# Performance work log

Measured on AMD Instinct MI355X. Metric: run time of the kernel, lower is better.

## Reference

```python
import jax, jax.numpy as jnp
import numpy as np

B, S, E, H = 2, 2048, 1024, 16
DH = E // H            # 64 head dim
ROT = DH // 2          # 32: RotaryEmbedding(head_dim//2) rotates first 32 dims only
CTX = 2048             # sliding KV window
THETA = 10000.0


def setup_inputs() -> dict:
    key = jax.random.key(0)
    ks = jax.random.split(key, 7)
    sc = 1.0 / np.sqrt(E)
    mk = lambda k, sh, s=1.0: (jax.random.normal(k, sh, jnp.float32) * s)
    return {
        "query": mk(ks[0], (B, S, E)),
        "key":   mk(ks[1], (B, S, E)),
        "value": mk(ks[2], (B, S, E)),
        "Wq": mk(ks[3], (E, E), sc), "bq": jnp.zeros((E,), jnp.float32),
        "Wk": mk(ks[4], (E, E), sc), "bk": jnp.zeros((E,), jnp.float32),
        "Wv": mk(ks[5], (E, E), sc), "bv": jnp.zeros((E,), jnp.float32),
        "Wo": mk(ks[6], (E, E), sc), "bo": jnp.zeros((E,), jnp.float32),
    }


def _rope(t):
    # t: [B, H, S, DH]; rotate first ROT dims, pass the rest through (offset=0).
    seq = t.shape[2]
    inv_freq = 1.0 / (THETA ** (jnp.arange(0, ROT, 2, dtype=jnp.float32) / ROT))  # [ROT//2]
    ang = jnp.arange(seq, dtype=jnp.float32)[:, None] * inv_freq[None, :]          # [S, ROT//2]
    cos = jnp.repeat(jnp.cos(ang), 2, axis=-1)  # [S, ROT] (pairwise-interleaved freqs)
    sin = jnp.repeat(jnp.sin(ang), 2, axis=-1)
    rot, rest = t[..., :ROT], t[..., ROT:]
    x1, x2 = rot[..., 0::2], rot[..., 1::2]
    rot_half = jnp.stack([-x2, x1], axis=-1).reshape(rot.shape)  # rotate_half on pairs
    return jnp.concatenate([rot * cos + rot_half * sin, rest], axis=-1)


def reference(query, key, value, Wq, bq, Wk, bk, Wv, bv, Wo, bo):
    def heads(x, W, b):
        return (x @ W.T + b).reshape(B, -1, H, DH).transpose(0, 2, 1, 3)  # [B,H,S,DH]

    q = _rope(heads(query, Wq, bq))
    k = _rope(heads(key, Wk, bk))
    v = heads(value, Wv, bv)
    k, v = k[:, :, -CTX:], v[:, :, -CTX:]  # sliding window (no-op when S == CTX)

    scale = jnp.float32(1.0 / np.sqrt(DH))
    scores = jnp.einsum('bhqd,bhkd->bhqk', q, k) * scale  # [B,H,Sq,Sk]
    sq, sk = q.shape[2], k.shape[2]
    causal = jnp.tril(jnp.ones((sk, sk), dtype=bool))[-sq:]  # [Sq,Sk]
    scores = jnp.where(causal[None, None], scores, jnp.float32(-jnp.inf))
    probs = jax.nn.softmax(scores, axis=-1)  # dropout=0 (eval)
    out = jnp.einsum('bhqk,bhkd->bhqd', probs, v)
    out = out.transpose(0, 2, 1, 3).reshape(B, -1, E)
    return out @ Wo.T + bo
```

## Files before the change

### kernel.cpp

```cpp
#include <hip/hip_runtime.h>
#include <stdint.h>
#include <math.h>

typedef __bf16 bf16x8 __attribute__((ext_vector_type(8)));
typedef float f32x4 __attribute__((ext_vector_type(4)));

__device__ __forceinline__ float bf2f(uint16_t x) {
  unsigned u = ((unsigned)x) << 16;
  float f;
  __builtin_memcpy(&f, &u, 4);
  return f;
}
__device__ __forceinline__ uint16_t f2bf(float f) {
  __bf16 h = (__bf16)f;
  uint16_t u;
  __builtin_memcpy(&u, &h, 2);
  return u;
}
__device__ __forceinline__ bf16x8 cvt8(const float* p) {
  const float4 lo = *(const float4*)p;
  const float4 hi = *(const float4*)(p + 4);
  bf16x8 v;
  v[0] = (__bf16)lo.x; v[1] = (__bf16)lo.y; v[2] = (__bf16)lo.z; v[3] = (__bf16)lo.w;
  v[4] = (__bf16)hi.x; v[5] = (__bf16)hi.y; v[6] = (__bf16)hi.z; v[7] = (__bf16)hi.w;
  return v;
}

typedef __attribute__((address_space(1))) const unsigned int gu32;
typedef __attribute__((address_space(3))) unsigned int lu32;
__device__ __forceinline__ void async_copy16(const void* gp, void* lp) {
  __builtin_amdgcn_global_load_lds((gu32*)gp, (lu32*)lp, 16, 0, 0);
}

__global__ __launch_bounds__(256) void cvt_kernel(
    const float* __restrict__ s0, uint16_t* __restrict__ d0,
    const float* __restrict__ s1, uint16_t* __restrict__ d1,
    const float* __restrict__ s2, uint16_t* __restrict__ d2) {
  const int z = blockIdx.z;
  const float* s = z == 0 ? s0 : z == 1 ? s1 : s2;
  uint16_t* d = z == 0 ? d0 : z == 1 ? d1 : d2;
  const size_t idx = ((size_t)blockIdx.x * 256 + threadIdx.x) * 8;
  *(bf16x8*)(d + idx) = cvt8(s + idx);
}

template <bool A_F32, bool W_F32, bool C_F32, bool VT>
__global__ __launch_bounds__(256) void gemm3_kernel(
    const void* __restrict__ A0, const void* __restrict__ W0,
    const float* __restrict__ b0, void* __restrict__ C0,
    const void* __restrict__ A1, const void* __restrict__ W1,
    const float* __restrict__ b1, void* __restrict__ C1,
    const void* __restrict__ A2, const void* __restrict__ W2,
    const float* __restrict__ b2, void* __restrict__ C2,
    int M, int N, int K) {
  const int z = blockIdx.z;
  const void* Av = z == 0 ? A0 : z == 1 ? A1 : A2;
  const void* Wp = z == 0 ? W0 : z == 1 ? W1 : W2;
  const float* bias = z == 0 ? b0 : z == 1 ? b1 : b2;
  void* Cv = z == 0 ? C0 : z == 1 ? C1 : C2;

  __shared__ __align__(16) uint16_t As[128 * 64];
  __shared__ __align__(16) uint16_t Bs[128 * 64];
  const int tid = threadIdx.x;
  const int wave = tid >> 6, lane = tid & 63;
  const int quad = lane >> 4, l16 = lane & 15;
  const int l = blockIdx.y * 8 + blockIdx.x;
  const int bn = (l >> 5) << 7;
  const int bm = (l & 31) << 7;
  const int wm = (wave >> 1) << 6, wn = (wave & 1) << 6;

  f32x4 acc[4][4] = {};

  for (int k0 = 0; k0 < K; k0 += 64) {
    bf16x8 ar[4], wr[4];
    if (A_F32) {
#pragma unroll
      for (int i = 0; i < 4; i++) {
        const int c = i * 256 + tid;
        const int r = c >> 3, pc = ((c & 7) ^ (r & 7)) << 3;
        ar[i] = cvt8((const float*)Av + (size_t)(bm + r) * K + k0 + pc);
      }
    }
    if (W_F32) {
#pragma unroll
      for (int i = 0; i < 4; i++) {
        const int c = i * 256 + tid;
        const int r = c >> 3, pc = ((c & 7) ^ (r & 7)) << 3;
        wr[i] = cvt8((const float*)Wp + (size_t)(bn + r) * K + k0 + pc);
      }
    }
    if (k0) __syncthreads();
#pragma unroll
    for (int i = 0; i < 4; i++) {
      const int c = i * 256 + tid;
      const int r = c >> 3, pc = ((c & 7) ^ (r & 7)) << 3;
      if (A_F32) *(bf16x8*)(As + c * 8) = ar[i];
      else async_copy16((const uint16_t*)Av + (size_t)(bm + r) * K + k0 + pc,
                        As + (i * 256 + (tid & 192)) * 8);
      if (W_F32) *(bf16x8*)(Bs + c * 8) = wr[i];
      else async_copy16((const uint16_t*)Wp + (size_t)(bn + r) * K + k0 + pc,
                        Bs + (i * 256 + (tid & 192)) * 8);
    }
    __syncthreads();
#pragma unroll
    for (int s = 0; s < 2; s++) {
      bf16x8 af[4], bfr[4];
#pragma unroll
      for (int i = 0; i < 4; i++) {
        const int Ra = wm + i * 16 + l16;
        af[i]  = *(const bf16x8*)(As + Ra * 64 + (((s * 4 + quad) ^ (Ra & 7)) << 3));
        const int Rb = wn + i * 16 + l16;
        bfr[i] = *(const bf16x8*)(Bs + Rb * 64 + (((s * 4 + quad) ^ (Rb & 7)) << 3));
      }
#pragma unroll
      for (int i = 0; i < 4; i++)
#pragma unroll
        for (int j = 0; j < 4; j++)
          acc[i][j] = __builtin_amdgcn_mfma_f32_16x16x32_bf16(af[i], bfr[j], acc[i][j], 0, 0, 0);
    }
  }
  if (VT && z == 2) {
#pragma unroll
    for (int j = 0; j < 4; j++) {
      const int n = bn + wn + j * 16 + l16;
      const float bj = bias[n];
      const int h = n >> 6, dh = n & 63;
#pragma unroll
      for (int i = 0; i < 4; i++) {
        const int m0 = bm + wm + i * 16 + quad * 4;
        const int b = m0 >> 11, s0 = m0 & 2047;
        uint2 pk;
        pk.x = (unsigned)f2bf(acc[i][j][0] + bj) |
               ((unsigned)f2bf(acc[i][j][1] + bj) << 16);
        pk.y = (unsigned)f2bf(acc[i][j][2] + bj) |
               ((unsigned)f2bf(acc[i][j][3] + bj) << 16);
        *(uint2*)((uint16_t*)Cv + ((size_t)((b * 16 + h) * 64 + dh)) * 2048 + s0) = pk;
      }
    }
  } else {
#pragma unroll
    for (int j = 0; j < 4; j++) {
      const int n = bn + wn + j * 16 + l16;
      const float bj = bias[n];
#pragma unroll
      for (int i = 0; i < 4; i++) {
        const int m0 = bm + wm + i * 16 + quad * 4;
#pragma unroll
        for (int r = 0; r < 4; r++) {
          const float v = acc[i][j][r] + bj;
          if (C_F32) ((float*)Cv)[(size_t)(m0 + r) * N + n] = v;
          else       ((uint16_t*)Cv)[(size_t)(m0 + r) * N + n] = f2bf(v);
        }
      }
    }
  }
}

__global__ __launch_bounds__(256) void rope_kernel(uint16_t* __restrict__ Q,
                                                   uint16_t* __restrict__ K) {
  const int tid = blockIdx.x * 256 + threadIdx.x;
  const int i = tid & 15;
  const int h = (tid >> 4) & 15;
  const int s = (tid >> 8) & 2047;
  const int b = tid >> 19;
  const size_t base = ((size_t)(b * 2048 + s) * 1024) + h * 64 + 2 * i;
  const float inv = __expf(-0.5756462732485115f * (float)i);
  float rev = ((float)s * inv) * 0.15915494309189535f;
  rev -= floorf(rev);
  const float sn = __builtin_amdgcn_sinf(rev);
  const float c  = __builtin_amdgcn_cosf(rev);
  {
    uint32_t p = *(const uint32_t*)(Q + base);
    float x0 = bf2f((uint16_t)p), x1 = bf2f((uint16_t)(p >> 16));
    *(uint32_t*)(Q + base) = (unsigned)f2bf(x0 * c - x1 * sn) |
                             ((unsigned)f2bf(x1 * c + x0 * sn) << 16);
  }
  {
    uint32_t p = *(const uint32_t*)(K + base);
    float x0 = bf2f((uint16_t)p), x1 = bf2f((uint16_t)(p >> 16));
    *(uint32_t*)(K + base) = (unsigned)f2bf(x0 * c - x1 * sn) |
                             ((unsigned)f2bf(x1 * c + x0 * sn) << 16);
  }
}

__global__ __launch_bounds__(256) void flash_kernel(const uint16_t* __restrict__ Q,
                                                    const uint16_t* __restrict__ K,
                                                    const uint16_t* __restrict__ VT,
                                                    uint16_t* __restrict__ AO) {
  const int bx = blockIdx.x;
  const int xcd = bx & 7;
  const int slot = bx >> 3;
  const int bh = (slot >> 5) * 8 + xcd;
  const int qt = 31 - (slot & 31);
  const int h = bh & 15;
  const int b = bh >> 4;
  const int tid = threadIdx.x;
  const int wave = tid >> 6, lane = tid & 63;
  const int quad = lane >> 4, l16 = lane & 15;

  __shared__ __align__(16) uint16_t Ks[64 * 64];
  __shared__ __align__(16) uint16_t Vt[64 * 64];
  __shared__ __align__(16) uint16_t Ps[4][16 * 72];

  const int qrow = qt * 64 + wave * 16 + l16;
  const size_t qoff = ((size_t)(b * 2048 + qrow) * 1024) + h * 64;
  bf16x8 qf[2];
#pragma unroll
  for (int s = 0; s < 2; s++) {
    union { bf16x8 v; uint16_t u[8]; } t;
    t.v = *(const bf16x8*)(Q + qoff + s * 32 + quad * 8);
#pragma unroll
    for (int j = 0; j < 8; j++) t.u[j] = f2bf(bf2f(t.u[j]) * 0.125f);
    qf[s] = t.v;
  }

  const size_t vbase = ((size_t)((b * 16 + h) * 64)) * 2048;

  float lsum = 0.f;
  f32x4 o[4] = {};

  const int nkt = qt + 1;
  for (int kt = 0; kt < nkt; kt++) {
    if (kt) __syncthreads();
#pragma unroll
    for (int i = 0; i < 2; i++) {
      const int c = i * 256 + tid;
      const int r = c >> 3, pc = ((c & 7) ^ (r & 7)) << 3;
      async_copy16(K + ((size_t)(b * 2048 + kt * 64 + r) * 1024) + h * 64 + pc,
                   Ks + (i * 256 + (tid & 192)) * 8);
      async_copy16(VT + vbase + (size_t)r * 2048 + kt * 64 + pc,
                   Vt + (i * 256 + (tid & 192)) * 8);
    }
    __syncthreads();

    f32x4 sacc[4] = {};
#pragma unroll
    for (int s = 0; s < 2; s++) {
#pragma unroll
      for (int t = 0; t < 4; t++) {
        const int R = t * 16 + l16;
        bf16x8 kf = *(const bf16x8*)(Ks + R * 64 + (((s * 4 + quad) ^ (R & 7)) << 3));
        sacc[t] = __builtin_amdgcn_mfma_f32_16x16x32_bf16(kf, qf[s], sacc[t], 0, 0, 0);
      }
    }
    if (kt == qt) {
      const int qg = qt * 64 + wave * 16 + l16;
#pragma unroll
      for (int t = 0; t < 4; t++)
#pragma unroll
        for (int r = 0; r < 4; r++) {
          const int kg = kt * 64 + t * 16 + quad * 4 + r;
          if (kg > qg) sacc[t][r] = -1e30f;
        }
    }
#pragma unroll
    for (int t = 0; t < 4; t++) {
      float p0 = __expf(sacc[t][0]), p1 = __expf(sacc[t][1]);
      float p2 = __expf(sacc[t][2]), p3 = __expf(sacc[t][3]);
      lsum += (p0 + p1) + (p2 + p3);
      uint2 pk;
      pk.x = (unsigned)f2bf(p0) | ((unsigned)f2bf(p1) << 16);
      pk.y = (unsigned)f2bf(p2) | ((unsigned)f2bf(p3) << 16);
      *(uint2*)(&Ps[wave][l16 * 72 + t * 16 + quad * 4]) = pk;
    }
#pragma unroll
    for (int s = 0; s < 2; s++) {
      const bf16x8 pa = *(const bf16x8*)(&Ps[wave][l16 * 72 + s * 32 + quad * 8]);
#pragma unroll
      for (int t = 0; t < 4; t++) {
        const int R = t * 16 + l16;
        const bf16x8 vb = *(const bf16x8*)(Vt + R * 64 + (((s * 4 + quad) ^ (R & 7)) << 3));
        o[t] = __builtin_amdgcn_mfma_f32_16x16x32_bf16(pa, vb, o[t], 0, 0, 0);
      }
    }
  }
  lsum += __shfl_xor(lsum, 16);
  lsum += __shfl_xor(lsum, 32);
  const float inv = 1.f / lsum;
  float invr[4];
#pragma unroll
  for (int r = 0; r < 4; r++) invr[r] = __shfl(inv, quad * 4 + r);
#pragma unroll
  for (int t = 0; t < 4; t++)
#pragma unroll
    for (int r = 0; r < 4; r++) {
      const int qg = qt * 64 + wave * 16 + quad * 4 + r;
      AO[((size_t)(b * 2048 + qg) * 1024) + h * 64 + t * 16 + l16] =
          f2bf(o[t][r] * invr[r]);
    }
}

extern "C" void kernel_launch(void* const* d_in, const int* in_sizes, int n_in,
                              void* d_out, int out_size, void* d_ws, size_t ws_size,
                              hipStream_t stream) {
  const float* query = (const float*)d_in[0];
  const float* key   = (const float*)d_in[1];
  const float* value = (const float*)d_in[2];
  const float* Wq = (const float*)d_in[3];
  const float* bq = (const float*)d_in[4];
  const float* Wk = (const float*)d_in[5];
  const float* bk = (const float*)d_in[6];
  const float* Wv = (const float*)d_in[7];
  const float* bv = (const float*)d_in[8];
  const float* Wo = (const float*)d_in[9];
  const float* bo = (const float*)d_in[10];
  float* out = (float*)d_out;

  uint16_t* ws = (uint16_t*)d_ws;
  uint16_t* Qb  = ws;
  uint16_t* Kb  = ws + (size_t)4194304;
  uint16_t* VTb = ws + (size_t)8388608;
  uint16_t* AOb = ws + (size_t)12582912;
  uint16_t* Wqc = AOb;
  uint16_t* Wkc = AOb + (size_t)1048576;
  uint16_t* Wvc = AOb + (size_t)2097152;

  dim3 blk(256);
  cvt_kernel<<<dim3(512, 1, 3), blk, 0, stream>>>(Wq, Wqc, Wk, Wkc, Wv, Wvc);
  gemm3_kernel<true, false, false, true><<<dim3(8, 32, 3), blk, 0, stream>>>(
      query, Wqc, bq, Qb,
      key,   Wkc, bk, Kb,
      value, Wvc, bv, VTb,
      4096, 1024, 1024);
  rope_kernel<<<dim3(4096), blk, 0, stream>>>(Qb, Kb);
  flash_kernel<<<dim3(1024), blk, 0, stream>>>(Qb, Kb, VTb, AOb);
  gemm3_kernel<false, true, true, false><<<dim3(8, 32, 1), blk, 0, stream>>>(
      AOb, Wo, bo, out,
      AOb, Wo, bo, out,
      AOb, Wo, bo, out,
      4096, 1024, 1024);
}
```

Before: 255.5 us.

## Fuse RoPE into projection GEMM epilogue and process two query tiles per flash block

RoPE is now applied inside the Q/K projection GEMM epilogue using a lane shuffle to fetch the paired element, which removes the separate rope kernel and its read-modify-write pass over Q and K. The flash kernel now handles two 64-row query tiles per block (rows qt2*128 and +64), sharing each K/V tile load between them, and the grid is halved. This cuts K/V global traffic and sync overhead per query row, at the cost of more registers and fewer blocks. The ROPE flag is also set on the V projection; this is only safe if the VT epilogue path never applies rotation, since rotating V would give wrong results.

```diff
diff --git a/kernel.cpp b/kernel.cpp
--- a/kernel.cpp
+++ b/kernel.cpp
@@ -43,7 +43,7 @@
   *(bf16x8*)(d + idx) = cvt8(s + idx);
 }
 
-template <bool A_F32, bool W_F32, bool C_F32, bool VT>
+template <bool A_F32, bool W_F32, bool C_F32, bool VT, bool ROPE>
 __global__ __launch_bounds__(256) void gemm3_kernel(
     const void* __restrict__ A0, const void* __restrict__ W0,
     const float* __restrict__ b0, void* __restrict__ C0,
@@ -141,44 +141,32 @@
     for (int j = 0; j < 4; j++) {
       const int n = bn + wn + j * 16 + l16;
       const float bj = bias[n];
+      const int dh = (wn + j * 16 + l16) & 63;
+      const bool rot = ROPE && (j < 2);
+      float invrev = 0.f;
+      if (rot)
+        invrev = __expf(-0.5756462732485115f * (float)(dh >> 1)) *
+                 0.15915494309189535f;
 #pragma unroll
       for (int i = 0; i < 4; i++) {
         const int m0 = bm + wm + i * 16 + quad * 4;
 #pragma unroll
         for (int r = 0; r < 4; r++) {
-          const float v = acc[i][j][r] + bj;
+          float v = acc[i][j][r] + bj;
+          if (rot) {
+            const int s_pos = (m0 + r) & 2047;
+            float rev = (float)s_pos * invrev;
+            rev -= floorf(rev);
+            const float sn = __builtin_amdgcn_sinf(rev);
+            const float cs = __builtin_amdgcn_cosf(rev);
+            const float partner = __shfl_xor(v, 1);
+            v = (dh & 1) ? (v * cs + partner * sn) : (v * cs - partner * sn);
+          }
           if (C_F32) ((float*)Cv)[(size_t)(m0 + r) * N + n] = v;
           else       ((uint16_t*)Cv)[(size_t)(m0 + r) * N + n] = f2bf(v);
         }
       }
     }
-  }
-}
-
-__global__ __launch_bounds__(256) void rope_kernel(uint16_t* __restrict__ Q,
-                                                   uint16_t* __restrict__ K) {
-  const int tid = blockIdx.x * 256 + threadIdx.x;
-  const int i = tid & 15;
-  const int h = (tid >> 4) & 15;
-  const int s = (tid >> 8) & 2047;
-  const int b = tid >> 19;
-  const size_t base = ((size_t)(b * 2048 + s) * 1024) + h * 64 + 2 * i;
-  const float inv = __expf(-0.5756462732485115f * (float)i);
-  float rev = ((float)s * inv) * 0.15915494309189535f;
-  rev -= floorf(rev);
-  const float sn = __builtin_amdgcn_sinf(rev);
-  const float c  = __builtin_amdgcn_cosf(rev);
-  {
-    uint32_t p = *(const uint32_t*)(Q + base);
-    float x0 = bf2f((uint16_t)p), x1 = bf2f((uint16_t)(p >> 16));
-    *(uint32_t*)(Q + base) = (unsigned)f2bf(x0 * c - x1 * sn) |
-                             ((unsigned)f2bf(x1 * c + x0 * sn) << 16);
-  }
-  {
-    uint32_t p = *(const uint32_t*)(K + base);
-    float x0 = bf2f((uint16_t)p), x1 = bf2f((uint16_t)(p >> 16));
-    *(uint32_t*)(K + base) = (unsigned)f2bf(x0 * c - x1 * sn) |
-                             ((unsigned)f2bf(x1 * c + x0 * sn) << 16);
   }
 }
 
@@ -189,8 +177,8 @@
   const int bx = blockIdx.x;
   const int xcd = bx & 7;
   const int slot = bx >> 3;
-  const int bh = (slot >> 5) * 8 + xcd;
-  const int qt = 31 - (slot & 31);
+  const int bh = (slot >> 4) * 8 + xcd;
+  const int qt2 = 15 - (slot & 15);
   const int h = bh & 15;
   const int b = bh >> 4;
   const int tid = threadIdx.x;
@@ -199,26 +187,31 @@
 
   __shared__ __align__(16) uint16_t Ks[64 * 64];
   __shared__ __align__(16) uint16_t Vt[64 * 64];
-  __shared__ __align__(16) uint16_t Ps[4][16 * 72];
-
-  const int qrow = qt * 64 + wave * 16 + l16;
-  const size_t qoff = ((size_t)(b * 2048 + qrow) * 1024) + h * 64;
-  bf16x8 qf[2];
+  __shared__ __align__(16) uint16_t Ps[4][32 * 72];
+
+  const int qrow0 = qt2 * 128 + wave * 16 + l16;
+  const int qrow1 = qrow0 + 64;
+  bf16x8 qf0[2], qf1[2];
 #pragma unroll
   for (int s = 0; s < 2; s++) {
-    union { bf16x8 v; uint16_t u[8]; } t;
-    t.v = *(const bf16x8*)(Q + qoff + s * 32 + quad * 8);
-#pragma unroll
-    for (int j = 0; j < 8; j++) t.u[j] = f2bf(bf2f(t.u[j]) * 0.125f);
-    qf[s] = t.v;
+    union { bf16x8 v; uint16_t u[8]; } t0, t1;
+    t0.v = *(const bf16x8*)(Q + ((size_t)(b * 2048 + qrow0) * 1024) + h * 64 + s * 32 + quad * 8);
+    t1.v = *(const bf16x8*)(Q + ((size_t)(b * 2048 + qrow1) * 1024) + h * 64 + s * 32 + quad * 8);
+#pragma unroll
+    for (int j = 0; j < 8; j++) {
+      t0.u[j] = f2bf(bf2f(t0.u[j]) * 0.125f);
+      t1.u[j] = f2bf(bf2f(t1.u[j]) * 0.125f);
+    }
+    qf0[s] = t0.v;
+    qf1[s] = t1.v;
   }
 
   const size_t vbase = ((size_t)((b * 16 + h) * 64)) * 2048;
 
-  float lsum = 0.f;
-  f32x4 o[4] = {};
-
-  const int nkt = qt + 1;
+  float lsum0 = 0.f, lsum1 = 0.f;
+  f32x4 o0[4] = {}, o1[4] = {};
+
+  const int nkt = 2 * qt2 + 2;
   for (int kt = 0; kt < nkt; kt++) {
     if (kt) __syncthreads();
 #pragma unroll
@@ -232,60 +225,107 @@
     }
     __syncthreads();
 
-    f32x4 sacc[4] = {};
+    const bool f0 = (kt < nkt - 1);
+
+    {
+      f32x4 sacc[4] = {};
+#pragma unroll
+      for (int s = 0; s < 2; s++)
+#pragma unroll
+        for (int t = 0; t < 4; t++) {
+          const int R = t * 16 + l16;
+          bf16x8 kf = *(const bf16x8*)(Ks + R * 64 + (((s * 4 + quad) ^ (R & 7)) << 3));
+          sacc[t] = __builtin_amdgcn_mfma_f32_16x16x32_bf16(kf, qf1[s], sacc[t], 0, 0, 0);
+        }
+      if (kt == nkt - 1) {
+#pragma unroll
+        for (int t = 0; t < 4; t++)
+#pragma unroll
+          for (int r = 0; r < 4; r++)
+            if (kt * 64 + t * 16 + quad * 4 + r > qrow1) sacc[t][r] = -1e30f;
+      }
+#pragma unroll
+      for (int t = 0; t < 4; t++) {
+        float p0 = __expf(sacc[t][0]), p1 = __expf(sacc[t][1]);
+        float p2 = __expf(sacc[t][2]), p3 = __expf(sacc[t][3]);
+        lsum1 += (p0 + p1) + (p2 + p3);
+        uint2 pk;
+        pk.x = (unsigned)f2bf(p0) | ((unsigned)f2bf(p1) << 16);
+        pk.y = (unsigned)f2bf(p2) | ((unsigned)f2bf(p3) << 16);
+        *(uint2*)(&Ps[wave][(16 + l16) * 72 + t * 16 + quad * 4]) = pk;
+      }
+    }
+    if (f0) {
+      f32x4 sacc[4] = {};
+#pragma unroll
+      for (int s = 0; s < 2; s++)
+#pragma unroll
+        for (int t = 0; t < 4; t++) {
+          const int R = t * 16 + l16;
+          bf16x8 kf = *(const bf16x8*)(Ks + R * 64 + (((s * 4 + quad) ^ (R & 7)) << 3));
+          sacc[t] = __builtin_amdgcn_mfma_f32_16x16x32_bf16(kf, qf0[s], sacc[t], 0, 0, 0);
+        }
+      if (kt == nkt - 2) {
+#pragma unroll
+        for (int t = 0; t < 4; t++)
+#pragma unroll
+          for (int r = 0; r < 4; r++)
+            if (kt * 64 + t * 16 + quad * 4 + r > qrow0) sacc[t][r] = -1e30f;
+      }
+#pragma unroll
+      for (int t = 0; t < 4; t++) {
+        float p0 = __expf(sacc[t][0]), p1 = __expf(sacc[t][1]);
+        float p2 = __expf(sacc[t][2]), p3 = __expf(sacc[t][3]);
+        lsum0 += (p0 + p1) + (p2 + p3);
+        uint2 pk;
+        pk.x = (unsigned)f2bf(p0) | ((unsigned)f2bf(p1) << 16);
+        pk.y = (unsigned)f2bf(p2) | ((unsigned)f2bf(p3) << 16);
+        *(uint2*)(&Ps[wave][l16 * 72 + t * 16 + quad * 4]) = pk;
+      }
+    }
 #pragma unroll
     for (int s = 0; s < 2; s++) {
-#pragma unroll
-      for (int t = 0; t < 4; t++) {
-        const int R = t * 16 + l16;
-        bf16x8 kf = *(const bf16x8*)(Ks + R * 64 + (((s * 4 + quad) ^ (R & 7)) << 3));
-        sacc[t] = __builtin_amdgcn_mfma_f32_16x16x32_bf16(kf, qf[s], sacc[t], 0, 0, 0);
-      }
-    }
-    if (kt == qt) {
-      const int qg = qt * 64 + wave * 16 + l16;
-#pragma unroll
-      for (int t = 0; t < 4; t++)
-#pragma unroll
-        for (int r = 0; r < 4; r++) {
-          const int kg = kt * 64 + t * 16 + quad * 4 + r;
-          if (kg > qg) sacc[t][r] = -1e30f;
-        }
-    }
-#pragma unroll
-    for (int t = 0; t < 4; t++) {
-      float p0 = __expf(sacc[t][0]), p1 = __expf(sacc[t][1]);
-      float p2 = __expf(sacc[t][2]), p3 = __expf(sacc[t][3]);
-      lsum += (p0 + p1) + (p2 + p3);
-      uint2 pk;
-      pk.x = (unsigned)f2bf(p0) | ((unsigned)f2bf(p1) << 16);
-      pk.y = (unsigned)f2bf(p2) | ((unsigned)f2bf(p3) << 16);
-      *(uint2*)(&Ps[wave][l16 * 72 + t * 16 + quad * 4]) = pk;
-    }
-#pragma unroll
-    for (int s = 0; s < 2; s++) {
-      const bf16x8 pa = *(const bf16x8*)(&Ps[wave][l16 * 72 + s * 32 + quad * 8]);
+      const bf16x8 pa1 = *(const bf16x8*)(&Ps[wave][(16 + l16) * 72 + s * 32 + quad * 8]);
 #pragma unroll
       for (int t = 0; t < 4; t++) {
         const int R = t * 16 + l16;
         const bf16x8 vb = *(const bf16x8*)(Vt + R * 64 + (((s * 4 + quad) ^ (R & 7)) << 3));
-        o[t] = __builtin_amdgcn_mfma_f32_16x16x32_bf16(pa, vb, o[t], 0, 0, 0);
-      }
-    }
-  }
-  lsum += __shfl_xor(lsum, 16);
-  lsum += __shfl_xor(lsum, 32);
-  const float inv = 1.f / lsum;
-  float invr[4];
-#pragma unroll
-  for (int r = 0; r < 4; r++) invr[r] = __shfl(inv, quad * 4 + r);
+        o1[t] = __builtin_amdgcn_mfma_f32_16x16x32_bf16(pa1, vb, o1[t], 0, 0, 0);
+      }
+    }
+    if (f0) {
+#pragma unroll
+      for (int s = 0; s < 2; s++) {
+        const bf16x8 pa0 = *(const bf16x8*)(&Ps[wave][l16 * 72 + s * 32 + quad * 8]);
+#pragma unroll
+        for (int t = 0; t < 4; t++) {
+          const int R = t * 16 + l16;
+          const bf16x8 vb = *(const bf16x8*)(Vt + R * 64 + (((s * 4 + quad) ^ (R & 7)) << 3));
+          o0[t] = __builtin_amdgcn_mfma_f32_16x16x32_bf16(pa0, vb, o0[t], 0, 0, 0);
+        }
+      }
+    }
+  }
+  lsum0 += __shfl_xor(lsum0, 16);
+  lsum0 += __shfl_xor(lsum0, 32);
+  lsum1 += __shfl_xor(lsum1, 16);
+  lsum1 += __shfl_xor(lsum1, 32);
+  const float inv0 = 1.f / lsum0, inv1 = 1.f / lsum1;
+  float invr0[4], invr1[4];
+#pragma unroll
+  for (int r = 0; r < 4; r++) {
+    invr0[r] = __shfl(inv0, quad * 4 + r);
+    invr1[r] = __shfl(inv1, quad * 4 + r);
+  }
 #pragma unroll
   for (int t = 0; t < 4; t++)
 #pragma unroll
     for (int r = 0; r < 4; r++) {
-      const int qg = qt * 64 + wave * 16 + quad * 4 + r;
-      AO[((size_t)(b * 2048 + qg) * 1024) + h * 64 + t * 16 + l16] =
-          f2bf(o[t][r] * invr[r]);
+      const int qg0 = qt2 * 128 + wave * 16 + quad * 4 + r;
+      AO[((size_t)(b * 2048 + qg0) * 1024) + h * 64 + t * 16 + l16] =
+          f2bf(o0[t][r] * invr0[r]);
+      AO[((size_t)(b * 2048 + qg0 + 64) * 1024) + h * 64 + t * 16 + l16] =
+          f2bf(o1[t][r] * invr1[r]);
     }
 }
 
@@ -316,14 +356,13 @@
 
   dim3 blk(256);
   cvt_kernel<<<dim3(512, 1, 3), blk, 0, stream>>>(Wq, Wqc, Wk, Wkc, Wv, Wvc);
-  gemm3_kernel<true, false, false, true><<<dim3(8, 32, 3), blk, 0, stream>>>(
+  gemm3_kernel<true, false, false, true, true><<<dim3(8, 32, 3), blk, 0, stream>>>(
       query, Wqc, bq, Qb,
       key,   Wkc, bk, Kb,
       value, Wvc, bv, VTb,
       4096, 1024, 1024);
-  rope_kernel<<<dim3(4096), blk, 0, stream>>>(Qb, Kb);
-  flash_kernel<<<dim3(1024), blk, 0, stream>>>(Qb, Kb, VTb, AOb);
-  gemm3_kernel<false, true, true, false><<<dim3(8, 32, 1), blk, 0, stream>>>(
+  flash_kernel<<<dim3(512), blk, 0, stream>>>(Qb, Kb, VTb, AOb);
+  gemm3_kernel<false, true, true, false, false><<<dim3(8, 32, 1), blk, 0, stream>>>(
       AOb, Wo, bo, out,
       AOb, Wo, bo, out,
       AOb, Wo, bo, out,
```

Result: no change. 250.7 us (-1.9%).
